# Kernel optimization log

Measured on AMD Instinct MI355X. Metric: run time of the kernel, lower is better.

## Reference

```python
import jax, jax.numpy as jnp
import numpy as np

B = 1048576
INDIM = 10
DIM = 32
LAYERS = 4
MODES = DIM // 2 + 1  # 17 rfft modes


def setup_inputs() -> dict:
    key = jax.random.key(0)
    ks = jax.random.split(key, 10)
    scale = 1.0 / (DIM * DIM)
    inp = {
        "x": jax.random.normal(ks[0], (B, INDIM), dtype=jnp.float32),
        # stem: Linear(indim, dim), stored as [in, out]
        "stem_W": jax.random.normal(ks[1], (INDIM, DIM), dtype=jnp.float32) / np.sqrt(INDIM),
        "stem_b": jnp.zeros((DIM,), dtype=jnp.float32),
        # per-layer complex spectral weights, stored as real/imag parts [L, modes, modes]
        "fno_wr": scale * jax.random.uniform(ks[2], (LAYERS, MODES, MODES), dtype=jnp.float32),
        "fno_wi": scale * jax.random.uniform(ks[3], (LAYERS, MODES, MODES), dtype=jnp.float32),
        # per-layer proj: Linear(dim, dim), stored as [L, in, out]
        "proj_W": jax.random.normal(ks[4], (LAYERS, DIM, DIM), dtype=jnp.float32) / np.sqrt(DIM),
        "proj_b": jnp.zeros((LAYERS, DIM), dtype=jnp.float32),
        # head: Linear(dim, indim)
        "head_W": jax.random.normal(ks[5], (DIM, INDIM), dtype=jnp.float32) / np.sqrt(DIM),
        "head_b": jnp.zeros((INDIM,), dtype=jnp.float32),
    }
    return inp


def reference(x, stem_W, stem_b, fno_wr, fno_wi, proj_W, proj_b, head_W, head_b):
    # stem
    h = x @ stem_W + stem_b  # [B, DIM]
    for i in range(LAYERS):
        w = fno_wr[i] + 1j * fno_wi[i]  # [MODES, MODES] complex64
        hf = jnp.fft.rfft(h, axis=-1)  # [B, MODES] complex
        # complex linear mix of modes (bias=False since condition_num=0)
        x1 = jnp.fft.irfft(jnp.einsum('bi,io->bo', hf, w), axis=-1)  # [B, DIM]
        x2 = h @ proj_W[i] + proj_b[i]  # [B, DIM]
        h = jax.nn.silu(x1 + x2)
    return h @ head_W + head_b  # [B, INDIM]
```

## Files before the change

kernel.cpp:

```cpp
#include <hip/hip_runtime.h>
#include <math.h>

#define INDIM 10
#define DIM 32
#define LAYERS 4
#define MODES 17

#define LOG2E 1.4426950408889634f
#define LN2   0.6931471805599453f

#define WS_FRAG_OFF 0
#define WS_BIAS_OFF 11264

typedef _Float16 f16;
typedef _Float16 f16x8 __attribute__((ext_vector_type(8)));
typedef float f32x16 __attribute__((ext_vector_type(16)));
typedef unsigned u32x2 __attribute__((ext_vector_type(2)));

union BU { f16x8 v; unsigned u[4]; };
union CU { f32x16 v; float4 q[4]; };

__global__ void fno_prep(const float* __restrict__ wr,
                         const float* __restrict__ wi,
                         const float* __restrict__ projW,
                         const float* __restrict__ stemW,
                         const float* __restrict__ headW,
                         const float* __restrict__ stemB,
                         const float* __restrict__ projB,
                         const float* __restrict__ headB,
                         f16* __restrict__ frag,
                         float* __restrict__ bias2) {
    const int l  = blockIdx.x;
    const int tx = threadIdx.x;
    const int j  = tx & 31;
    const int n  = tx >> 5;

    __shared__ float ct[32], st[32];
    __shared__ float sre[MODES][32], sim[MODES][32];
    if (tx < 32) {
        float ang = (2.0f * 3.14159265358979323846f / 32.0f) * (float)tx;
        ct[tx] = cosf(ang);
        st[tx] = sinf(ang);
    }
    __syncthreads();

    const float* lwr = wr + l * MODES * MODES;
    const float* lwi = wi + l * MODES * MODES;

    if (tx < MODES * 32) {
        const int o  = tx >> 5;
        const int nn = tx & 31;
        float re = 0.0f, im = 0.0f;
        for (int m = 0; m < MODES; ++m) {
            int t = (m * nn) & 31;
            float c = ct[t], s = st[t];
            float a = lwr[m * MODES + o];
            float b = lwi[m * MODES + o];
            re += c * a + s * b;
            im += c * b - s * a;
        }
        sre[o][nn] = re;
        sim[o][nn] = im;
    }
    __syncthreads();

    float acc = 0.0f;
    for (int o = 0; o < MODES; ++o) {
        int t2 = (o * j) & 31;
        float f = (o == 0 || o == 16) ? 1.0f : 2.0f;
        acc += f * (sre[o][n] * ct[t2] - sim[o][n] * st[t2]);
    }
    acc = acc * (1.0f / 32.0f) + projW[(l * DIM + n) * DIM + j];

    const float wscale = (l == 0) ? LOG2E : 1.0f;
    const int kc = n >> 4;
    const int G  = (n >> 3) & 1;
    const int e  = n & 7;
    const int ln = G * 32 + j;
    frag[((l * 2 + kc) * 64 + ln) * 8 + e] = (f16)(wscale * acc);

    if (l == 0) {
        if (tx < 64) {
            const int lnn = tx;
            const int c2  = lnn & 31;
            const int G2  = lnn >> 5;
#pragma unroll
            for (int ee = 0; ee < 8; ++ee) {
                int k = 8 * G2 + ee;
                frag[(8 * 64 + lnn) * 8 + ee] =
                    (f16)(k < INDIM ? stemW[k * DIM + c2] : 0.0f);
            }
#pragma unroll
            for (int kcc = 0; kcc < 2; ++kcc)
#pragma unroll
                for (int ee = 0; ee < 8; ++ee) {
                    int k = 16 * kcc + 8 * G2 + ee;
                    frag[((9 + kcc) * 64 + lnn) * 8 + ee] =
                        (f16)(c2 < INDIM ? LN2 * headW[k * INDIM + c2] : 0.0f);
                }
        }
        if (tx < 32) {
#pragma unroll
            for (int f = 0; f < 6; ++f) {
                float v;
                if (f == 0)      v = stemB[tx];
                else if (f <= 4) v = LOG2E * projB[(f - 1) * DIM + tx];
                else             v = (tx < INDIM) ? headB[tx] : 0.0f;
                bias2[f * 32 + tx] = v;
            }
        }
    }
}

__device__ __forceinline__ float exp2_fast(float x) {
#if __has_builtin(__builtin_amdgcn_exp2f)
    return __builtin_amdgcn_exp2f(x);
#else
    return exp2f(x);
#endif
}

__device__ __forceinline__ unsigned pk2(float a, float b) {
    auto h2 = __builtin_amdgcn_cvt_pkrtz(a, b);
    return __builtin_bit_cast(unsigned, h2);
}

__device__ __forceinline__ void pswap(unsigned& a, unsigned& b) {
#if __has_builtin(__builtin_amdgcn_permlane32_swap)
    u32x2 r = __builtin_amdgcn_permlane32_swap(a, b, false, false);
    a = r[0];
    b = r[1];
#else
    asm("v_permlane32_swap_b32 %0, %1" : "+v"(a), "+v"(b));
    __builtin_amdgcn_sched_barrier(0);
#endif
}

template <bool SILU>
__device__ __forceinline__ void pack_exchange(const f32x16& D, BU& b0, BU& b1) {
    unsigned q[8];
#pragma unroll
    for (int h = 0; h < 2; ++h) {
        float u[8];
        if (SILU) {
#pragma unroll
            for (int r = 0; r < 8; ++r) u[r] = exp2_fast(-D[8 * h + r]);
#pragma unroll
            for (int r = 0; r < 8; ++r) u[r] = 1.0f + u[r];
#pragma unroll
            for (int r = 0; r < 8; ++r) u[r] = __builtin_amdgcn_rcpf(u[r]);
#pragma unroll
            for (int r = 0; r < 8; ++r) u[r] = D[8 * h + r] * u[r];
        } else {
#pragma unroll
            for (int r = 0; r < 8; ++r) u[r] = D[8 * h + r];
        }
        q[4 * h + 0] = pk2(u[0], u[1]);
        q[4 * h + 1] = pk2(u[2], u[3]);
        q[4 * h + 2] = pk2(u[4], u[5]);
        q[4 * h + 3] = pk2(u[6], u[7]);
    }
    pswap(q[0], q[2]);
    pswap(q[1], q[3]);
    pswap(q[4], q[6]);
    pswap(q[5], q[7]);
    b0.u[0] = q[0]; b0.u[1] = q[1]; b0.u[2] = q[2]; b0.u[3] = q[3];
    b1.u[0] = q[4]; b1.u[1] = q[5]; b1.u[2] = q[6]; b1.u[3] = q[7];
}

__device__ __forceinline__ f32x16 ld_bias(const float* sbias, int stage, int G) {
    CU c;
#pragma unroll
    for (int rq = 0; rq < 4; ++rq)
        c.q[rq] = *(const float4*)&sbias[stage * 32 + rq * 8 + G * 4];
    return c.v;
}

__device__ __forceinline__ f16x8 ld_frag(const f16* sfrag, int f, int ln) {
    return *(const f16x8*)&sfrag[(f * 64 + ln) * 8];
}

template <bool GUARD>
__device__ __forceinline__ BU load_x(const float* __restrict__ x, long rb,
                                     int c, int G, int nrows) {
    BU b;
    b.u[0] = 0; b.u[1] = 0; b.u[2] = 0; b.u[3] = 0;
    const long r = rb + c;
    if (!GUARD || r < nrows) {
        const float* xp = x + r * INDIM;
        if (G == 0) {
            float2 p0 = *(const float2*)(xp + 0);
            float2 p1 = *(const float2*)(xp + 2);
            float2 p2 = *(const float2*)(xp + 4);
            float2 p3 = *(const float2*)(xp + 6);
            b.u[0] = pk2(p0.x, p0.y);
            b.u[1] = pk2(p1.x, p1.y);
            b.u[2] = pk2(p2.x, p2.y);
            b.u[3] = pk2(p3.x, p3.y);
        } else {
            float2 p4 = *(const float2*)(xp + 8);
            b.u[0] = pk2(p4.x, p4.y);
        }
    }
    return b;
}

template <bool GUARD>
__device__ __forceinline__ void store_o(float* __restrict__ out, long rb,
                                        int c, int G, int nrows, const f32x16& Dh) {
    const long r = rb + c;
    if (!GUARD || r < nrows) {
        float* op = out + r * INDIM;
        if (G == 0) {
            *(float2*)(op + 0) = make_float2(Dh[0], Dh[1]);
            *(float2*)(op + 2) = make_float2(Dh[2], Dh[3]);
            *(float2*)(op + 8) = make_float2(Dh[4], Dh[5]);
        } else {
            *(float2*)(op + 4) = make_float2(Dh[0], Dh[1]);
            *(float2*)(op + 6) = make_float2(Dh[2], Dh[3]);
        }
    }
}

template <bool GUARD>
__global__ __launch_bounds__(256, 8) void fno_main(
    const float* __restrict__ x,
    const f16*  __restrict__ fragbuf,
    const float* __restrict__ bias2,
    float* __restrict__ out,
    int nrows) {

    __shared__ __align__(16) f16 sfrag[11 * 64 * 8];
    __shared__ __align__(16) float sbias[6 * 32];

    {
        const int tid = threadIdx.x;
        uint4* dv = (uint4*)sfrag;
        const uint4* sv = (const uint4*)fragbuf;
#pragma unroll
        for (int i = 0; i < 3; ++i) {
            int idx = tid + i * 256;
            if (idx < 704) dv[idx] = sv[idx];
        }
        if (tid < 48) ((float4*)sbias)[tid] = ((const float4*)bias2)[tid];
    }
    __syncthreads();

    const int tid = threadIdx.x;
    const int w   = tid >> 6;
    const int ln  = tid & 63;
    const int c   = ln & 31;
    const int G   = ln >> 5;

    const long rb = (long)blockIdx.x * 128 + (long)w * 32;

    BU bx = load_x<GUARD>(x, rb, c, G, nrows);
    f16x8 as = ld_frag(sfrag, 8, ln);
    f32x16 cb = ld_bias(sbias, 0, G);
    f32x16 D = __builtin_amdgcn_mfma_f32_32x32x16_f16(as, bx.v, cb, 0, 0, 0);

    BU b0, b1;
    pack_exchange<false>(D, b0, b1);

#pragma unroll
    for (int l = 0; l < LAYERS; ++l) {
        f16x8 w0 = ld_frag(sfrag, 2 * l, ln);
        f16x8 w1 = ld_frag(sfrag, 2 * l + 1, ln);
        cb = ld_bias(sbias, 1 + l, G);
        f32x16 t = __builtin_amdgcn_mfma_f32_32x32x16_f16(w0, b0.v, cb, 0, 0, 0);
        t = __builtin_amdgcn_mfma_f32_32x32x16_f16(w1, b1.v, t, 0, 0, 0);
        pack_exchange<true>(t, b0, b1);
    }

    f16x8 ah0 = ld_frag(sfrag, 9, ln);
    f16x8 ah1 = ld_frag(sfrag, 10, ln);
    cb = ld_bias(sbias, 5, G);
    f32x16 H = __builtin_amdgcn_mfma_f32_32x32x16_f16(ah0, b0.v, cb, 0, 0, 0);
    H = __builtin_amdgcn_mfma_f32_32x32x16_f16(ah1, b1.v, H, 0, 0, 0);

    store_o<GUARD>(out, rb, c, G, nrows, H);
}

extern "C" void kernel_launch(void* const* d_in, const int* in_sizes, int n_in,
                              void* d_out, int out_size, void* d_ws, size_t ws_size,
                              hipStream_t stream) {
    const float* x      = (const float*)d_in[0];
    const float* stemW  = (const float*)d_in[1];
    const float* stemB  = (const float*)d_in[2];
    const float* fno_wr = (const float*)d_in[3];
    const float* fno_wi = (const float*)d_in[4];
    const float* projW  = (const float*)d_in[5];
    const float* projB  = (const float*)d_in[6];
    const float* headW  = (const float*)d_in[7];
    const float* headB  = (const float*)d_in[8];
    float* out = (float*)d_out;

    f16*   frag  = (f16*)((char*)d_ws + WS_FRAG_OFF);
    float* bias2 = (float*)((char*)d_ws + WS_BIAS_OFF);

    const int nrows = in_sizes[0] / INDIM;

    fno_prep<<<LAYERS, 1024, 0, stream>>>(fno_wr, fno_wi, projW, stemW, headW,
                                          stemB, projB, headB, frag, bias2);

    const int rows_per_block = 128;
    const int nblk = (nrows + rows_per_block - 1) / rows_per_block;
    if (nrows % rows_per_block == 0)
        fno_main<false><<<nblk, 256, 0, stream>>>(x, frag, bias2, out, nrows);
    else
        fno_main<true><<<nblk, 256, 0, stream>>>(x, frag, bias2, out, nrows);
}
```

Baseline: 50.11 us.

## Switch from 32x32x16 to 16x16x32 MFMA tiles with 16 rows per wave

The fused FNO-MLP kernel now uses 16x16x32 f16 MFMAs instead of 32x32x16, so each wave handles 16 rows rather than 32. The prep kernel re-lays the weight fragments to match, and the head layer shrinks to a single MFMA because K=32 fits one instruction. Activations are re-fragmented with a permlane32 swap followed by a permlane16 swap. The aim is fewer wasted MFMA cycles on the padded stem and head and less per-wave latency, at the cost of twice as many blocks and the prologue copying shared-memory fragments more often per row.

```diff
diff --git a/kernel.cpp b/kernel.cpp
--- a/kernel.cpp
+++ b/kernel.cpp
@@ -14,11 +14,10 @@
 
 typedef _Float16 f16;
 typedef _Float16 f16x8 __attribute__((ext_vector_type(8)));
-typedef float f32x16 __attribute__((ext_vector_type(16)));
+typedef float f32x4v __attribute__((ext_vector_type(4)));
 typedef unsigned u32x2 __attribute__((ext_vector_type(2)));
 
 union BU { f16x8 v; unsigned u[4]; };
-union CU { f32x16 v; float4 q[4]; };
 
 __global__ void fno_prep(const float* __restrict__ wr,
                          const float* __restrict__ wi,
@@ -73,31 +72,30 @@
     acc = acc * (1.0f / 32.0f) + projW[(l * DIM + n) * DIM + j];
 
     const float wscale = (l == 0) ? LOG2E : 1.0f;
-    const int kc = n >> 4;
-    const int G  = (n >> 3) & 1;
+    const int h  = j >> 4;
+    const int ln = 16 * (n >> 3) + (j & 15);
     const int e  = n & 7;
-    const int ln = G * 32 + j;
-    frag[((l * 2 + kc) * 64 + ln) * 8 + e] = (f16)(wscale * acc);
+    frag[((l * 2 + h) * 64 + ln) * 8 + e] = (f16)(wscale * acc);
 
     if (l == 0) {
         if (tx < 64) {
             const int lnn = tx;
-            const int c2  = lnn & 31;
-            const int G2  = lnn >> 5;
+            const int c2  = lnn & 15;
+            const int g2  = lnn >> 4;
+#pragma unroll
+            for (int hh = 0; hh < 2; ++hh)
+#pragma unroll
+                for (int ee = 0; ee < 8; ++ee) {
+                    int k = 8 * g2 + ee;
+                    frag[((8 + hh) * 64 + lnn) * 8 + ee] =
+                        (f16)(k < INDIM ? stemW[k * DIM + 16 * hh + c2] : 0.0f);
+                }
 #pragma unroll
             for (int ee = 0; ee < 8; ++ee) {
-                int k = 8 * G2 + ee;
-                frag[(8 * 64 + lnn) * 8 + ee] =
-                    (f16)(k < INDIM ? stemW[k * DIM + c2] : 0.0f);
+                int k = 8 * g2 + ee;
+                frag[(10 * 64 + lnn) * 8 + ee] =
+                    (f16)(c2 < INDIM ? LN2 * headW[k * INDIM + c2] : 0.0f);
             }
-#pragma unroll
-            for (int kcc = 0; kcc < 2; ++kcc)
-#pragma unroll
-                for (int ee = 0; ee < 8; ++ee) {
-                    int k = 16 * kcc + 8 * G2 + ee;
-                    frag[((9 + kcc) * 64 + lnn) * 8 + ee] =
-                        (f16)(c2 < INDIM ? LN2 * headW[k * INDIM + c2] : 0.0f);
-                }
         }
         if (tx < 32) {
 #pragma unroll
@@ -125,7 +123,7 @@
     return __builtin_bit_cast(unsigned, h2);
 }
 
-__device__ __forceinline__ void pswap(unsigned& a, unsigned& b) {
+__device__ __forceinline__ void pswap32(unsigned& a, unsigned& b) {
 #if __has_builtin(__builtin_amdgcn_permlane32_swap)
     u32x2 r = __builtin_amdgcn_permlane32_swap(a, b, false, false);
     a = r[0];
@@ -136,44 +134,50 @@
 #endif
 }
 
+__device__ __forceinline__ void pswap16(unsigned& a, unsigned& b) {
+#if __has_builtin(__builtin_amdgcn_permlane16_swap)
+    u32x2 r = __builtin_amdgcn_permlane16_swap(a, b, false, false);
+    a = r[0];
+    b = r[1];
+#else
+    asm("v_permlane16_swap_b32 %0, %1" : "+v"(a), "+v"(b));
+    __builtin_amdgcn_sched_barrier(0);
+#endif
+}
+
 template <bool SILU>
-__device__ __forceinline__ void pack_exchange(const f32x16& D, BU& b0, BU& b1) {
-    unsigned q[8];
-#pragma unroll
-    for (int h = 0; h < 2; ++h) {
+__device__ __forceinline__ void pack_exchange16(const f32x4v& D0, const f32x4v& D1,
+                                                BU& b) {
+    float s[8];
+    if (SILU) {
         float u[8];
-        if (SILU) {
-#pragma unroll
-            for (int r = 0; r < 8; ++r) u[r] = exp2_fast(-D[8 * h + r]);
-#pragma unroll
-            for (int r = 0; r < 8; ++r) u[r] = 1.0f + u[r];
-#pragma unroll
-            for (int r = 0; r < 8; ++r) u[r] = __builtin_amdgcn_rcpf(u[r]);
-#pragma unroll
-            for (int r = 0; r < 8; ++r) u[r] = D[8 * h + r] * u[r];
-        } else {
-#pragma unroll
-            for (int r = 0; r < 8; ++r) u[r] = D[8 * h + r];
-        }
-        q[4 * h + 0] = pk2(u[0], u[1]);
-        q[4 * h + 1] = pk2(u[2], u[3]);
-        q[4 * h + 2] = pk2(u[4], u[5]);
-        q[4 * h + 3] = pk2(u[6], u[7]);
-    }
-    pswap(q[0], q[2]);
-    pswap(q[1], q[3]);
-    pswap(q[4], q[6]);
-    pswap(q[5], q[7]);
-    b0.u[0] = q[0]; b0.u[1] = q[1]; b0.u[2] = q[2]; b0.u[3] = q[3];
-    b1.u[0] = q[4]; b1.u[1] = q[5]; b1.u[2] = q[6]; b1.u[3] = q[7];
-}
-
-__device__ __forceinline__ f32x16 ld_bias(const float* sbias, int stage, int G) {
-    CU c;
-#pragma unroll
-    for (int rq = 0; rq < 4; ++rq)
-        c.q[rq] = *(const float4*)&sbias[stage * 32 + rq * 8 + G * 4];
-    return c.v;
+#pragma unroll
+        for (int r = 0; r < 4; ++r) { u[r] = exp2_fast(-D0[r]); u[4 + r] = exp2_fast(-D1[r]); }
+#pragma unroll
+        for (int r = 0; r < 8; ++r) u[r] = 1.0f + u[r];
+#pragma unroll
+        for (int r = 0; r < 8; ++r) u[r] = __builtin_amdgcn_rcpf(u[r]);
+#pragma unroll
+        for (int r = 0; r < 4; ++r) { s[r] = D0[r] * u[r]; s[4 + r] = D1[r] * u[4 + r]; }
+    } else {
+#pragma unroll
+        for (int r = 0; r < 4; ++r) { s[r] = D0[r]; s[4 + r] = D1[r]; }
+    }
+    unsigned P0 = pk2(s[0], s[1]);
+    unsigned P1 = pk2(s[2], s[3]);
+    unsigned Q0 = pk2(s[4], s[5]);
+    unsigned Q1 = pk2(s[6], s[7]);
+    pswap32(P0, Q0);
+    pswap32(P1, Q1);
+    pswap16(P0, Q0);
+    pswap16(P1, Q1);
+    b.u[0] = P0; b.u[1] = P1; b.u[2] = Q0; b.u[3] = Q1;
+}
+
+__device__ __forceinline__ f32x4v ld_bias4(const float* sbias, int stage, int h, int g) {
+    float4 q = *(const float4*)&sbias[stage * 32 + 16 * h + 4 * g];
+    f32x4v v = {q.x, q.y, q.z, q.w};
+    return v;
 }
 
 __device__ __forceinline__ f16x8 ld_frag(const f16* sfrag, int f, int ln) {
@@ -182,13 +186,13 @@
 
 template <bool GUARD>
 __device__ __forceinline__ BU load_x(const float* __restrict__ x, long rb,
-                                     int c, int G, int nrows) {
+                                     int c, int g, int nrows) {
     BU b;
     b.u[0] = 0; b.u[1] = 0; b.u[2] = 0; b.u[3] = 0;
     const long r = rb + c;
     if (!GUARD || r < nrows) {
         const float* xp = x + r * INDIM;
-        if (G == 0) {
+        if (g == 0) {
             float2 p0 = *(const float2*)(xp + 0);
             float2 p1 = *(const float2*)(xp + 2);
             float2 p2 = *(const float2*)(xp + 4);
@@ -197,7 +201,7 @@
             b.u[1] = pk2(p1.x, p1.y);
             b.u[2] = pk2(p2.x, p2.y);
             b.u[3] = pk2(p3.x, p3.y);
-        } else {
+        } else if (g == 1) {
             float2 p4 = *(const float2*)(xp + 8);
             b.u[0] = pk2(p4.x, p4.y);
         }
@@ -207,17 +211,18 @@
 
 template <bool GUARD>
 __device__ __forceinline__ void store_o(float* __restrict__ out, long rb,
-                                        int c, int G, int nrows, const f32x16& Dh) {
+                                        int c, int g, int nrows, const f32x4v& H) {
     const long r = rb + c;
     if (!GUARD || r < nrows) {
         float* op = out + r * INDIM;
-        if (G == 0) {
-            *(float2*)(op + 0) = make_float2(Dh[0], Dh[1]);
-            *(float2*)(op + 2) = make_float2(Dh[2], Dh[3]);
-            *(float2*)(op + 8) = make_float2(Dh[4], Dh[5]);
-        } else {
-            *(float2*)(op + 4) = make_float2(Dh[0], Dh[1]);
-            *(float2*)(op + 6) = make_float2(Dh[2], Dh[3]);
+        if (g == 0) {
+            *(float2*)(op + 0) = make_float2(H[0], H[1]);
+            *(float2*)(op + 2) = make_float2(H[2], H[3]);
+        } else if (g == 1) {
+            *(float2*)(op + 4) = make_float2(H[0], H[1]);
+            *(float2*)(op + 6) = make_float2(H[2], H[3]);
+        } else if (g == 2) {
+            *(float2*)(op + 8) = make_float2(H[0], H[1]);
         }
     }
 }
@@ -249,36 +254,33 @@
     const int tid = threadIdx.x;
     const int w   = tid >> 6;
     const int ln  = tid & 63;
-    const int c   = ln & 31;
-    const int G   = ln >> 5;
-
-    const long rb = (long)blockIdx.x * 128 + (long)w * 32;
-
-    BU bx = load_x<GUARD>(x, rb, c, G, nrows);
-    f16x8 as = ld_frag(sfrag, 8, ln);
-    f32x16 cb = ld_bias(sbias, 0, G);
-    f32x16 D = __builtin_amdgcn_mfma_f32_32x32x16_f16(as, bx.v, cb, 0, 0, 0);
-
-    BU b0, b1;
-    pack_exchange<false>(D, b0, b1);
+    const int c   = ln & 15;
+    const int g   = ln >> 4;
+
+    const long rb = (long)blockIdx.x * 64 + (long)w * 16;
+
+    BU bx = load_x<GUARD>(x, rb, c, g, nrows);
+    f16x8 as0 = ld_frag(sfrag, 8, ln);
+    f16x8 as1 = ld_frag(sfrag, 9, ln);
+    f32x4v D0 = __builtin_amdgcn_mfma_f32_16x16x32_f16(as0, bx.v, ld_bias4(sbias, 0, 0, g), 0, 0, 0);
+    f32x4v D1 = __builtin_amdgcn_mfma_f32_16x16x32_f16(as1, bx.v, ld_bias4(sbias, 0, 1, g), 0, 0, 0);
+
+    BU b;
+    pack_exchange16<false>(D0, D1, b);
 
 #pragma unroll
     for (int l = 0; l < LAYERS; ++l) {
         f16x8 w0 = ld_frag(sfrag, 2 * l, ln);
         f16x8 w1 = ld_frag(sfrag, 2 * l + 1, ln);
-        cb = ld_bias(sbias, 1 + l, G);
-        f32x16 t = __builtin_amdgcn_mfma_f32_32x32x16_f16(w0, b0.v, cb, 0, 0, 0);
-        t = __builtin_amdgcn_mfma_f32_32x32x16_f16(w1, b1.v, t, 0, 0, 0);
-        pack_exchange<true>(t, b0, b1);
-    }
-
-    f16x8 ah0 = ld_frag(sfrag, 9, ln);
-    f16x8 ah1 = ld_frag(sfrag, 10, ln);
-    cb = ld_bias(sbias, 5, G);
-    f32x16 H = __builtin_amdgcn_mfma_f32_32x32x16_f16(ah0, b0.v, cb, 0, 0, 0);
-    H = __builtin_amdgcn_mfma_f32_32x32x16_f16(ah1, b1.v, H, 0, 0, 0);
-
-    store_o<GUARD>(out, rb, c, G, nrows, H);
+        f32x4v t0 = __builtin_amdgcn_mfma_f32_16x16x32_f16(w0, b.v, ld_bias4(sbias, 1 + l, 0, g), 0, 0, 0);
+        f32x4v t1 = __builtin_amdgcn_mfma_f32_16x16x32_f16(w1, b.v, ld_bias4(sbias, 1 + l, 1, g), 0, 0, 0);
+        pack_exchange16<true>(t0, t1, b);
+    }
+
+    f16x8 ah = ld_frag(sfrag, 10, ln);
+    f32x4v H = __builtin_amdgcn_mfma_f32_16x16x32_f16(ah, b.v, ld_bias4(sbias, 5, 0, g), 0, 0, 0);
+
+    store_o<GUARD>(out, rb, c, g, nrows, H);
 }
 
 extern "C" void kernel_launch(void* const* d_in, const int* in_sizes, int n_in,
@@ -303,7 +305,7 @@
     fno_prep<<<LAYERS, 1024, 0, stream>>>(fno_wr, fno_wi, projW, stemW, headW,
                                           stemB, projB, headB, frag, bias2);
 
-    const int rows_per_block = 128;
+    const int rows_per_block = 64;
     const int nblk = (nrows + rows_per_block - 1) / rows_per_block;
     if (nrows % rows_per_block == 0)
         fno_main<false><<<nblk, 256, 0, stream>>>(x, frag, bias2, out, nrows);
```

Result: slower. 51.42 us (+2.6%).
